# Optimization experiments

Hardware: AMD Instinct MI355X
Metric: run time of the kernel (lower is better)

## Reference

```python
import jax, jax.numpy as jnp
import numpy as np

N_NODES = 50000
N_EDGES = 1600000
F_IN = 384
NR_SIGMOID = 1  # hidden_sizes[-1]


def setup_inputs() -> dict:
    key = jax.random.key(0)
    ks = jax.random.split(key, 8)
    x = jax.random.normal(ks[0], (N_NODES, F_IN), jnp.float32)
    edge_index = jax.random.randint(ks[1], (2, N_EDGES), 0, N_NODES, jnp.int32)
    def lin(k, fin, fout):
        return jax.random.normal(k, (fin, fout), jnp.float32) / np.sqrt(fin).astype(np.float32)
    W1 = lin(ks[2], F_IN, 64)
    W2 = lin(ks[3], 64, 32)
    W3 = lin(ks[4], 32, 1 + F_IN)  # reconstruction=True: last width = 1 + input_size
    return {
        "x": x, "edge_index": edge_index,
        "W1": W1, "b1": jnp.zeros((64,), jnp.float32),
        "W2": W2, "b2": jnp.zeros((32,), jnp.float32),
        "W3": W3, "b3": jnp.zeros((1 + F_IN,), jnp.float32),
    }


def reference(x, edge_index, W1, b1, W2, b2, W3, b3):
    N = x.shape[0]
    self_loop = jnp.arange(N, dtype=edge_index.dtype)
    src = jnp.concatenate([edge_index[0], self_loop])  # [E+N]
    dst = jnp.concatenate([edge_index[1], self_loop])
    # symmetric GCN normalization (with self-loops), as in PyG GCNConv
    deg = jax.ops.segment_sum(jnp.ones(dst.shape[0], x.dtype), dst, num_segments=N)
    dinv = jnp.where(deg > 0, jax.lax.rsqrt(deg), 0.0)
    norm = (dinv[src] * dinv[dst])[:, None]  # [E+N, 1]

    def gcn_conv(h, W, b):
        m = h @ W                         # transform first (fewer message bytes)
        agg = jax.ops.segment_sum(m[src] * norm, dst, num_segments=N)
        return agg + b

    h = jax.nn.relu(gcn_conv(x, W1, b1))
    h = jax.nn.relu(gcn_conv(h, W2, b2))
    h = gcn_conv(h, W3, b3)
    # sigmoid on the first nr_sigmoid_layers columns only
    return jnp.concatenate([jax.nn.sigmoid(h[:, :NR_SIGMOID]), h[:, NR_SIGMOID:]], axis=1)
```

## Files before the change

### kernel.cpp

```cpp
#include <hip/hip_runtime.h>

#define F_IN  384
#define EPB   4096
#define NBINS 256
#define BCAP  10240
#define SDS   208
#define WTBLK 144

typedef __attribute__((ext_vector_type(8))) short short8v;
typedef __attribute__((ext_vector_type(4))) float f32x4;

__device__ __forceinline__ unsigned short f2bf(float f) {
    unsigned u = __float_as_uint(f);
    return (unsigned short)((u + 0x7FFFu + ((u >> 16) & 1u)) >> 16);
}
__device__ __forceinline__ float bflo(unsigned u) { return __uint_as_float(u << 16); }
__device__ __forceinline__ float bfhi(unsigned u) { return __uint_as_float(u & 0xFFFF0000u); }


__launch_bounds__(256)
__global__ void k_p1(const int* __restrict__ ei, int E, int NBK, int NB1,
                     unsigned* __restrict__ packed, unsigned short* __restrict__ segdesc,
                     const float* __restrict__ W1, const float* __restrict__ W3,
                     unsigned short* __restrict__ w1t, unsigned short* __restrict__ w3t) {
    __shared__ unsigned sin[EPB];
    __shared__ unsigned sout[EPB];
    __shared__ int hist[257], cur[256], excl[257];
    const int t = threadIdx.x;

    if (blockIdx.x >= NB1) {
        int idx = (blockIdx.x - NB1) * 256 + t;
        if (idx < 384 * 64) {
            int k = idx >> 6, col = idx & 63;
            w1t[(size_t)col * 384 + k] = f2bf(W1[idx]);
        } else {
            int j = idx - 384 * 64;
            if (j < 384 * 32) {
                int col = j >> 5, k = j & 31;
                w3t[(size_t)col * 32 + k] = f2bf(W3[(size_t)k * 385 + col]);
            }
        }
        return;
    }

    const int e0 = blockIdx.x * EPB;
    const int cnt = min(EPB, E - e0);

    if (t < 256) { hist[t] = 0; cur[t] = 0; }
    if (t == 0) hist[256] = 0;
    __syncthreads();

    for (int i = t; i < cnt; i += 256) {
        int s = ei[e0 + i];
        int d = ei[E + e0 + i];
        sin[i] = ((unsigned)d << 16) | (unsigned)s;
        atomicAdd(&hist[d >> 8], 1);
    }
    __syncthreads();

    if (t < 64) {
        int carry = 0;
        for (int c = 0; c * 64 < NBK; ++c) {
            int idx = c * 64 + t;
            int v = (idx < NBK) ? hist[idx] : 0;
            int x = v;
#pragma unroll
            for (int d = 1; d < 64; d <<= 1) { int y = __shfl_up(x, d, 64); if (t >= d) x += y; }
            if (idx < NBK) excl[idx] = carry + x - v;
            carry += __shfl(x, 63, 64);
        }
        if (t == 0) excl[NBK] = carry;
    }
    __syncthreads();

    for (int i = t; i < cnt; i += 256) {
        unsigned v = sin[i];
        int b = v >> 24;
        int pos = excl[b] + atomicAdd(&cur[b], 1);
        sout[pos] = v;
    }
    __syncthreads();

    for (int i = t; i < cnt; i += 256) packed[(size_t)e0 + i] = sout[i];
    for (int i = t; i <= NBK; i += 256) segdesc[(size_t)blockIdx.x * SDS + i] = (unsigned short)excl[i];
}


__launch_bounds__(256)
__global__ void k_p2(const unsigned* __restrict__ packed, const unsigned short* __restrict__ segdesc,
                     int NB1, unsigned short* __restrict__ eidx,
                     int* __restrict__ rpB, int* __restrict__ rpE,
                     float* __restrict__ dinv, int N) {
    __shared__ unsigned ev[BCAP];
    __shared__ unsigned short se[BCAP];
    __shared__ int lenS[512], offS[513], srcS[512];
    __shared__ int hist[NBINS], cur[NBINS], excl[NBINS + 1];
    const int t = threadIdx.x;
    const int b = blockIdx.x;

    if (t < NBINS) { hist[t] = 0; cur[t] = 0; }
    for (int blk = t; blk < NB1; blk += 256) {
        int s0 = segdesc[(size_t)blk * SDS + b];
        int s1 = segdesc[(size_t)blk * SDS + b + 1];
        lenS[blk] = s1 - s0;
        srcS[blk] = s0;
    }
    __syncthreads();

    if (t < 64) {
        int carry = 0;
        for (int c = 0; c * 64 < NB1; ++c) {
            int idx = c * 64 + t;
            int v = (idx < NB1) ? lenS[idx] : 0;
            int x = v;
#pragma unroll
            for (int d = 1; d < 64; d <<= 1) { int y = __shfl_up(x, d, 64); if (t >= d) x += y; }
            if (idx < NB1) offS[idx] = carry + x - v;
            carry += __shfl(x, 63, 64);
        }
        if (t == 0) offS[NB1 < 512 ? NB1 : 512] = carry;
    }
    __syncthreads();
    const int total = min(offS[NB1 < 512 ? NB1 : 512], BCAP);

    for (int blk = t; blk < NB1; blk += 256) {
        int l = lenS[blk], o = offS[blk];
        if (o + l > BCAP) l = max(0, BCAP - o);
        const unsigned* sp = packed + (size_t)blk * EPB + srcS[blk];
        for (int j = 0; j < l; ++j) ev[o + j] = sp[j];
    }
    __syncthreads();

    for (int i = t; i < total; i += 256) atomicAdd(&hist[(ev[i] >> 16) & 0xFF], 1);
    __syncthreads();

    if (t < 64) {
        int carry = 0;
#pragma unroll
        for (int c = 0; c < 4; ++c) {
            int idx = c * 64 + t;
            int v = hist[idx];
            int x = v;
#pragma unroll
            for (int d = 1; d < 64; d <<= 1) { int y = __shfl_up(x, d, 64); if (t >= d) x += y; }
            excl[idx] = carry + x - v;
            carry += __shfl(x, 63, 64);
        }
        if (t == 0) excl[NBINS] = carry;
    }
    __syncthreads();

    if (t < NBINS) {
        int d = b * NBINS + t;
        if (d < N) {
            int c = hist[t];
            int base = b * BCAP + excl[t];
            rpB[d] = base;
            rpE[d] = base + c;
            dinv[d] = rsqrtf((float)(c + 1));
        }
    }
    for (int i = t; i < total; i += 256) {
        unsigned v = ev[i];
        int l = (v >> 16) & 0xFF;
        int p = excl[l] + atomicAdd(&cur[l], 1);
        se[p] = (unsigned short)(v & 0xFFFF);
    }
    __syncthreads();
    for (int i = t; i < total; i += 256) eidx[(size_t)b * BCAP + i] = se[i];
}


__launch_bounds__(256)
__global__ void k_gemm1(const float* __restrict__ x, const unsigned short* __restrict__ w1t,
                        const float* __restrict__ dinv,
                        unsigned short* __restrict__ m1p, int N) {
    __shared__ __align__(16) unsigned short xb[32][136];
    const int t    = threadIdx.x;
    const int lane = t & 63;
    const int wv   = t >> 6;
    const int lr   = lane & 15;
    const int kg   = lane >> 4;
    const int row0 = blockIdx.x * 32;
    const int col  = (wv << 4) + lr;

    short8v bf[12];
    const unsigned short* wcol = w1t + (size_t)col * 384 + (kg << 3);
#pragma unroll
    for (int c = 0; c < 12; c++)
        bf[c] = *reinterpret_cast<const short8v*>(&wcol[c * 32]);

    int sr[2], sk[2];
    const float* sp[2];
    bool sv[2];
#pragma unroll
    for (int i = 0; i < 2; i++) {
        int g = t + i * 256;
        sr[i] = g >> 4;
        sk[i] = (g & 15) << 3;
        int row = row0 + sr[i];
        sv[i] = (row < N);
        sp[i] = x + (size_t)row * F_IN + sk[i];
    }

    float4 preA0, preA1, preB0, preB1;
    preA0 = sv[0] ? *reinterpret_cast<const float4*>(sp[0])     : make_float4(0, 0, 0, 0);
    preA1 = sv[0] ? *reinterpret_cast<const float4*>(sp[0] + 4) : make_float4(0, 0, 0, 0);
    preB0 = sv[1] ? *reinterpret_cast<const float4*>(sp[1])     : make_float4(0, 0, 0, 0);
    preB1 = sv[1] ? *reinterpret_cast<const float4*>(sp[1] + 4) : make_float4(0, 0, 0, 0);

    f32x4 acc0 = (f32x4){0.f, 0.f, 0.f, 0.f};
    f32x4 acc1 = (f32x4){0.f, 0.f, 0.f, 0.f};

    for (int k0 = 0; k0 < F_IN; k0 += 128) {
        __syncthreads();
        {
            short8v p;
            p[0] = (short)f2bf(preA0.x); p[1] = (short)f2bf(preA0.y);
            p[2] = (short)f2bf(preA0.z); p[3] = (short)f2bf(preA0.w);
            p[4] = (short)f2bf(preA1.x); p[5] = (short)f2bf(preA1.y);
            p[6] = (short)f2bf(preA1.z); p[7] = (short)f2bf(preA1.w);
            *reinterpret_cast<short8v*>(&xb[sr[0]][sk[0]]) = p;
            p[0] = (short)f2bf(preB0.x); p[1] = (short)f2bf(preB0.y);
            p[2] = (short)f2bf(preB0.z); p[3] = (short)f2bf(preB0.w);
            p[4] = (short)f2bf(preB1.x); p[5] = (short)f2bf(preB1.y);
            p[6] = (short)f2bf(preB1.z); p[7] = (short)f2bf(preB1.w);
            *reinterpret_cast<short8v*>(&xb[sr[1]][sk[1]]) = p;
        }
        if (k0 + 128 < F_IN) {
            const float* q0 = sp[0] + k0 + 128;
            const float* q1 = sp[1] + k0 + 128;
            preA0 = sv[0] ? *reinterpret_cast<const float4*>(q0)     : make_float4(0, 0, 0, 0);
            preA1 = sv[0] ? *reinterpret_cast<const float4*>(q0 + 4) : make_float4(0, 0, 0, 0);
            preB0 = sv[1] ? *reinterpret_cast<const float4*>(q1)     : make_float4(0, 0, 0, 0);
            preB1 = sv[1] ? *reinterpret_cast<const float4*>(q1 + 4) : make_float4(0, 0, 0, 0);
        }
        __syncthreads();

#pragma unroll
        for (int kk = 0; kk < 4; kk++) {
            const int c = (k0 >> 5) + kk;
            short8v a0 = *reinterpret_cast<const short8v*>(&xb[lr][(kk << 5) + (kg << 3)]);
            short8v a1 = *reinterpret_cast<const short8v*>(&xb[16 + lr][(kk << 5) + (kg << 3)]);
            acc0 = __builtin_amdgcn_mfma_f32_16x16x32_bf16(a0, bf[c], acc0, 0, 0, 0);
            acc1 = __builtin_amdgcn_mfma_f32_16x16x32_bf16(a1, bf[c], acc1, 0, 0, 0);
        }
    }

    const size_t hbase = (size_t)(col >> 5) * ((size_t)N * 32) + (col & 31);
#pragma unroll
    for (int i = 0; i < 4; i++) {
        int rowA = row0 + (kg << 2) + i;
        if (rowA < N) m1p[hbase + (size_t)rowA * 32] = f2bf(acc0[i] * dinv[rowA]);
        int rowB = row0 + 16 + (kg << 2) + i;
        if (rowB < N) m1p[hbase + (size_t)rowB * 32] = f2bf(acc1[i] * dinv[rowB]);
    }
}


__launch_bounds__(256)
__global__ void k_g64half(const int* __restrict__ rpB, const int* __restrict__ rpE,
                          const unsigned short* __restrict__ eidx,
                          const unsigned* __restrict__ msg,
                          const float* __restrict__ b1h,
                          const float* __restrict__ dinv,
                          unsigned* __restrict__ m1h,
                          int houtoff, int N) {
    int w = blockIdx.x * 16 + (threadIdx.x >> 4);
    if (w >= N) return;
    int f = threadIdx.x & 15;
    int i = rpB[w], e = rpE[w];
    unsigned u = msg[(size_t)w * 16 + f];
    float l0 = bflo(u), h0 = bfhi(u);
    float l1 = 0.f, h1 = 0.f, l2 = 0.f, h2 = 0.f, l3 = 0.f, h3 = 0.f;
    float l4 = 0.f, h4 = 0.f, l5 = 0.f, h5 = 0.f, l6 = 0.f, h6 = 0.f, l7 = 0.f, h7 = 0.f;
    for (; i + 8 <= e; i += 8) {
        unsigned u0 = msg[(size_t)eidx[i]     * 16 + f];
        unsigned u1 = msg[(size_t)eidx[i + 1] * 16 + f];
        unsigned u2 = msg[(size_t)eidx[i + 2] * 16 + f];
        unsigned u3 = msg[(size_t)eidx[i + 3] * 16 + f];
        unsigned u4 = msg[(size_t)eidx[i + 4] * 16 + f];
        unsigned u5 = msg[(size_t)eidx[i + 5] * 16 + f];
        unsigned u6 = msg[(size_t)eidx[i + 6] * 16 + f];
        unsigned u7 = msg[(size_t)eidx[i + 7] * 16 + f];
        l0 += bflo(u0); h0 += bfhi(u0);  l1 += bflo(u1); h1 += bfhi(u1);
        l2 += bflo(u2); h2 += bfhi(u2);  l3 += bflo(u3); h3 += bfhi(u3);
        l4 += bflo(u4); h4 += bfhi(u4);  l5 += bflo(u5); h5 += bfhi(u5);
        l6 += bflo(u6); h6 += bfhi(u6);  l7 += bflo(u7); h7 += bfhi(u7);
    }
    for (; i + 4 <= e; i += 4) {
        unsigned u0 = msg[(size_t)eidx[i]     * 16 + f];
        unsigned u1 = msg[(size_t)eidx[i + 1] * 16 + f];
        unsigned u2 = msg[(size_t)eidx[i + 2] * 16 + f];
        unsigned u3 = msg[(size_t)eidx[i + 3] * 16 + f];
        l0 += bflo(u0); h0 += bfhi(u0);  l1 += bflo(u1); h1 += bfhi(u1);
        l2 += bflo(u2); h2 += bfhi(u2);  l3 += bflo(u3); h3 += bfhi(u3);
    }
    for (; i < e; i++) {
        unsigned u0 = msg[(size_t)eidx[i] * 16 + f];
        l0 += bflo(u0); h0 += bfhi(u0);
    }
    float suml = ((l0 + l1) + (l2 + l3)) + ((l4 + l5) + (l6 + l7));
    float sumh = ((h0 + h1) + (h2 + h3)) + ((h4 + h5) + (h6 + h7));
    float s = dinv[w];
    float hl = fmaxf(suml * s + b1h[(f << 1)], 0.f);
    float hh = fmaxf(sumh * s + b1h[(f << 1) + 1], 0.f);
    m1h[(size_t)w * 32 + houtoff + f] = (unsigned)f2bf(hl) | ((unsigned)f2bf(hh) << 16);
}


__launch_bounds__(256)
__global__ void k_gather32h(const int* __restrict__ rpB, const int* __restrict__ rpE,
                            const unsigned short* __restrict__ eidx,
                            const unsigned* __restrict__ msg,
                            unsigned* __restrict__ outp, int N,
                            const float* __restrict__ bias, const float* __restrict__ dinv) {
    int w = blockIdx.x * 16 + (threadIdx.x >> 4);
    if (w >= N) return;
    int f = threadIdx.x & 15;
    int i = rpB[w], e = rpE[w];
    unsigned u = msg[(size_t)w * 16 + f];
    float l0 = bflo(u), h0 = bfhi(u);
    float l1 = 0.f, h1 = 0.f, l2 = 0.f, h2 = 0.f, l3 = 0.f, h3 = 0.f;
    float l4 = 0.f, h4 = 0.f, l5 = 0.f, h5 = 0.f, l6 = 0.f, h6 = 0.f, l7 = 0.f, h7 = 0.f;
    for (; i + 8 <= e; i += 8) {
        unsigned u0 = msg[(size_t)eidx[i]     * 16 + f];
        unsigned u1 = msg[(size_t)eidx[i + 1] * 16 + f];
        unsigned u2 = msg[(size_t)eidx[i + 2] * 16 + f];
        unsigned u3 = msg[(size_t)eidx[i + 3] * 16 + f];
        unsigned u4 = msg[(size_t)eidx[i + 4] * 16 + f];
        unsigned u5 = msg[(size_t)eidx[i + 5] * 16 + f];
        unsigned u6 = msg[(size_t)eidx[i + 6] * 16 + f];
        unsigned u7 = msg[(size_t)eidx[i + 7] * 16 + f];
        l0 += bflo(u0); h0 += bfhi(u0);  l1 += bflo(u1); h1 += bfhi(u1);
        l2 += bflo(u2); h2 += bfhi(u2);  l3 += bflo(u3); h3 += bfhi(u3);
        l4 += bflo(u4); h4 += bfhi(u4);  l5 += bflo(u5); h5 += bfhi(u5);
        l6 += bflo(u6); h6 += bfhi(u6);  l7 += bflo(u7); h7 += bfhi(u7);
    }
    for (; i + 4 <= e; i += 4) {
        unsigned u0 = msg[(size_t)eidx[i]     * 16 + f];
        unsigned u1 = msg[(size_t)eidx[i + 1] * 16 + f];
        unsigned u2 = msg[(size_t)eidx[i + 2] * 16 + f];
        unsigned u3 = msg[(size_t)eidx[i + 3] * 16 + f];
        l0 += bflo(u0); h0 += bfhi(u0);  l1 += bflo(u1); h1 += bfhi(u1);
        l2 += bflo(u2); h2 += bfhi(u2);  l3 += bflo(u3); h3 += bfhi(u3);
    }
    for (; i < e; i++) {
        unsigned u0 = msg[(size_t)eidx[i] * 16 + f];
        l0 += bflo(u0); h0 += bfhi(u0);
    }
    float rl = ((l0 + l1) + (l2 + l3)) + ((l4 + l5) + (l6 + l7));
    float rh = ((h0 + h1) + (h2 + h3)) + ((h4 + h5) + (h6 + h7));
    float s = dinv[w];
    rl = fmaxf(rl * s + bias[(f << 1)], 0.f) * s;
    rh = fmaxf(rh * s + bias[(f << 1) + 1], 0.f) * s;
    outp[(size_t)w * 16 + f] = (unsigned)f2bf(rl) | ((unsigned)f2bf(rh) << 16);
}


__launch_bounds__(256)
__global__ void k_layer2(const unsigned* __restrict__ m1h, const float* __restrict__ W2,
                         const float* __restrict__ dinv,
                         unsigned short* __restrict__ m2p, int N) {
    const int t    = threadIdx.x;
    const int lane = t & 63;
    const int wv   = t >> 6;
    const int lr   = lane & 15;
    const int kg   = lane >> 4;
    const int row0 = blockIdx.x * 64 + (wv << 4);

    short8v b00, b01, b10, b11;
#pragma unroll
    for (int j = 0; j < 8; j++) {
        int k = (kg << 3) + j;
        b00[j] = (short)f2bf(W2[(size_t)k * 32 + lr]);
        b01[j] = (short)f2bf(W2[(size_t)k * 32 + 16 + lr]);
        b10[j] = (short)f2bf(W2[(size_t)(32 + k) * 32 + lr]);
        b11[j] = (short)f2bf(W2[(size_t)(32 + k) * 32 + 16 + lr]);
    }

    int arow = row0 + lr;
    short8v a0 = (short8v){0, 0, 0, 0, 0, 0, 0, 0};
    short8v a1 = (short8v){0, 0, 0, 0, 0, 0, 0, 0};
    if (arow < N) {
        a0 = *reinterpret_cast<const short8v*>(&m1h[(size_t)arow * 32 + (kg << 2)]);
        a1 = *reinterpret_cast<const short8v*>(&m1h[(size_t)arow * 32 + 16 + (kg << 2)]);
    }

    f32x4 accA = (f32x4){0.f, 0.f, 0.f, 0.f};
    f32x4 accB = (f32x4){0.f, 0.f, 0.f, 0.f};
    accA = __builtin_amdgcn_mfma_f32_16x16x32_bf16(a0, b00, accA, 0, 0, 0);
    accA = __builtin_amdgcn_mfma_f32_16x16x32_bf16(a1, b10, accA, 0, 0, 0);
    accB = __builtin_amdgcn_mfma_f32_16x16x32_bf16(a0, b01, accB, 0, 0, 0);
    accB = __builtin_amdgcn_mfma_f32_16x16x32_bf16(a1, b11, accB, 0, 0, 0);

#pragma unroll
    for (int i = 0; i < 4; i++) {
        int row = row0 + (kg << 2) + i;
        if (row < N) {
            float s = dinv[row];
            m2p[(size_t)row * 32 + lr]      = f2bf(accA[i] * s);
            m2p[(size_t)row * 32 + 16 + lr] = f2bf(accB[i] * s);
        }
    }
}


__launch_bounds__(256)
__global__ void k_g32out(const int* __restrict__ rpB, const int* __restrict__ rpE,
                         const unsigned short* __restrict__ eidx,
                         const uint4* __restrict__ msg,
                         const float* __restrict__ dinv,
                         const unsigned short* __restrict__ w3t,
                         const float* __restrict__ W3, const float* __restrict__ b3,
                         float* __restrict__ out, int N) {
    __shared__ unsigned g[64][16];
    const int t    = threadIdx.x;
    const int row0 = blockIdx.x * 64;
    const int wn   = t >> 2;
    const int q    = t & 3;
    const int w    = row0 + wn;

    if (w < N) {
        int i = rpB[w], e = rpE[w];
        uint4 u = msg[(size_t)w * 4 + q];
        float a0 = bflo(u.x), a1 = bfhi(u.x), a2 = bflo(u.y), a3 = bfhi(u.y);
        float a4 = bflo(u.z), a5 = bfhi(u.z), a6 = bflo(u.w), a7 = bfhi(u.w);
        float c0 = 0.f, c1 = 0.f, c2 = 0.f, c3 = 0.f, c4 = 0.f, c5 = 0.f, c6 = 0.f, c7 = 0.f;
        for (; i + 4 <= e; i += 4) {
            uint4 v0 = msg[(size_t)eidx[i]     * 4 + q];
            uint4 v1 = msg[(size_t)eidx[i + 1] * 4 + q];
            uint4 v2 = msg[(size_t)eidx[i + 2] * 4 + q];
            uint4 v3 = msg[(size_t)eidx[i + 3] * 4 + q];
            a0 += bflo(v0.x); a1 += bfhi(v0.x); a2 += bflo(v0.y); a3 += bfhi(v0.y);
            a4 += bflo(v0.z); a5 += bfhi(v0.z); a6 += bflo(v0.w); a7 += bfhi(v0.w);
            c0 += bflo(v1.x); c1 += bfhi(v1.x); c2 += bflo(v1.y); c3 += bfhi(v1.y);
            c4 += bflo(v1.z); c5 += bfhi(v1.z); c6 += bflo(v1.w); c7 += bfhi(v1.w);
            a0 += bflo(v2.x); a1 += bfhi(v2.x); a2 += bflo(v2.y); a3 += bfhi(v2.y);
            a4 += bflo(v2.z); a5 += bfhi(v2.z); a6 += bflo(v2.w); a7 += bfhi(v2.w);
            c0 += bflo(v3.x); c1 += bfhi(v3.x); c2 += bflo(v3.y); c3 += bfhi(v3.y);
            c4 += bflo(v3.z); c5 += bfhi(v3.z); c6 += bflo(v3.w); c7 += bfhi(v3.w);
        }
        for (; i < e; i++) {
            uint4 v0 = msg[(size_t)eidx[i] * 4 + q];
            a0 += bflo(v0.x); a1 += bfhi(v0.x); a2 += bflo(v0.y); a3 += bfhi(v0.y);
            a4 += bflo(v0.z); a5 += bfhi(v0.z); a6 += bflo(v0.w); a7 += bfhi(v0.w);
        }
        float s = dinv[w];
        float g0 = (a0 + c0) * s, g1 = (a1 + c1) * s, g2 = (a2 + c2) * s, g3 = (a3 + c3) * s;
        float g4 = (a4 + c4) * s, g5 = (a5 + c5) * s, g6 = (a6 + c6) * s, g7 = (a7 + c7) * s;
        g[wn][q * 4 + 0] = (unsigned)f2bf(g0) | ((unsigned)f2bf(g1) << 16);
        g[wn][q * 4 + 1] = (unsigned)f2bf(g2) | ((unsigned)f2bf(g3) << 16);
        g[wn][q * 4 + 2] = (unsigned)f2bf(g4) | ((unsigned)f2bf(g5) << 16);
        g[wn][q * 4 + 3] = (unsigned)f2bf(g6) | ((unsigned)f2bf(g7) << 16);
        const float* wc = W3 + (size_t)(8 * q) * 385 + 384;
        float p = g0 * wc[0] + g1 * wc[385] + g2 * wc[2 * 385] + g3 * wc[3 * 385]
                + g4 * wc[4 * 385] + g5 * wc[5 * 385] + g6 * wc[6 * 385] + g7 * wc[7 * 385];
        p += __shfl_xor(p, 1, 64);
        p += __shfl_xor(p, 2, 64);
        if (q == 0) out[(size_t)w * 385 + 384] = p + b3[384];
    } else {
        g[wn][q * 4 + 0] = 0; g[wn][q * 4 + 1] = 0;
        g[wn][q * 4 + 2] = 0; g[wn][q * 4 + 3] = 0;
    }
    __syncthreads();

    const int lane = t & 63;
    const int wv   = t >> 6;
    const int lr   = lane & 15;
    const int kg   = lane >> 4;
#pragma unroll
    for (int y = 0; y < 6; y++) {
        int col = y * 64 + (wv << 4) + lr;
        short8v bfrag = *reinterpret_cast<const short8v*>(&w3t[(size_t)col * 32 + (kg << 3)]);
        float bias = b3[col];
#pragma unroll
        for (int rb = 0; rb < 4; rb++) {
            short8v afrag = *reinterpret_cast<const short8v*>(&g[(rb << 4) + lr][kg << 2]);
            f32x4 acc = (f32x4){0.f, 0.f, 0.f, 0.f};
            acc = __builtin_amdgcn_mfma_f32_16x16x32_bf16(afrag, bfrag, acc, 0, 0, 0);
#pragma unroll
            for (int i = 0; i < 4; i++) {
                int row = row0 + (rb << 4) + (kg << 2) + i;
                if (row < N) {
                    float v = acc[i] + bias;
                    if (col == 0) v = 1.0f / (1.0f + expf(-v));
                    out[(size_t)row * 385 + col] = v;
                }
            }
        }
    }
}

extern "C" void kernel_launch(void* const* d_in, const int* in_sizes, int n_in,
                              void* d_out, int out_size, void* d_ws, size_t ws_size,
                              hipStream_t stream) {
    const float* x  = (const float*)d_in[0];
    const int*   ei = (const int*)d_in[1];
    const float* W1 = (const float*)d_in[2];
    const float* b1 = (const float*)d_in[3];
    const float* W2 = (const float*)d_in[4];
    const float* b2 = (const float*)d_in[5];
    const float* W3 = (const float*)d_in[6];
    const float* b3 = (const float*)d_in[7];
    float* out = (float*)d_out;

    const int N = in_sizes[0] / F_IN;
    const int E = in_sizes[1] / 2;
    const int NB1 = (E + EPB - 1) / EPB;
    const int NBK = (N + NBINS - 1) / NBINS;

    float* ws   = (float*)d_ws;
    float* dinv = ws;
    float* bufA = ws + N;
    float* bufB = bufA + (size_t)64 * N;
    int*   rpB  = (int*)(bufB + (size_t)64 * N);
    int*   rpE  = rpB + N;
    unsigned short* eidx    = (unsigned short*)(rpE + N);
    unsigned short* segdesc = eidx + (size_t)NBK * BCAP;
    unsigned short* w1t     = segdesc + (size_t)NB1 * SDS;
    unsigned short* w3t     = w1t + (size_t)64 * 384;

    unsigned* packed = (unsigned*)bufA;
    unsigned short* m1p = (unsigned short*)bufA;
    unsigned* m1h = (unsigned*)bufB;
    unsigned short* m2p = (unsigned short*)bufA;
    unsigned short* h2p = (unsigned short*)bufB;

    k_p1<<<NB1 + WTBLK, 256, 0, stream>>>(ei, E, NBK, NB1, packed, segdesc, W1, W3, w1t, w3t);
    k_p2<<<NBK, 256, 0, stream>>>(packed, segdesc, NB1, eidx, rpB, rpE, dinv, N);

    k_gemm1  <<<(N + 31) / 32, 256, 0, stream>>>(x, w1t, dinv, m1p, N);
    k_g64half<<<(N + 15) / 16, 256, 0, stream>>>(rpB, rpE, eidx,
                                                 (const unsigned*)m1p,                    b1,      dinv, m1h,  0, N);
    k_g64half<<<(N + 15) / 16, 256, 0, stream>>>(rpB, rpE, eidx,
                                                 (const unsigned*)(m1p + (size_t)N * 32), b1 + 32, dinv, m1h, 16, N);

    k_layer2  <<<(N + 63) / 64, 256, 0, stream>>>(m1h, W2, dinv, m2p, N);
    k_gather32h<<<(N + 15) / 16, 256, 0, stream>>>(rpB, rpE, eidx, (const unsigned*)m2p,
                                                   (unsigned*)h2p, N, b2, dinv);

    k_g32out<<<(N + 63) / 64, 256, 0, stream>>>(rpB, rpE, eidx, (const uint4*)h2p, dinv,
                                                w3t, W3, b3, out, N);
}
```

Measured before the change: 145.1 us.

## Fuse layer-1 GEMM into edge-partition kernel and apply dinv scaling in bucket pass

The x@W1 GEMM blocks now run in the same launch as the first edge-partition pass and the W3 transpose, so the GEMM overlaps with the sort work and one kernel launch disappears. W1 is converted to bf16 inline per thread instead of through a pre-transposed buffer. Because dinv is not yet available at that point, the second partition kernel rescales the bf16 GEMM output by dinv after computing degrees. That adds a read-modify-write pass over m1p and a second bf16 rounding, and m1p moves to a separate offset so it does not alias the packed edge buffer.

```diff
diff --git a/kernel.cpp b/kernel.cpp
--- a/kernel.cpp
+++ b/kernel.cpp
@@ -5,7 +5,7 @@
 #define NBINS 256
 #define BCAP  10240
 #define SDS   208
-#define WTBLK 144
+#define WT3B  48
 
 typedef __attribute__((ext_vector_type(8))) short short8v;
 typedef __attribute__((ext_vector_type(4))) float f32x4;
@@ -17,44 +17,125 @@
 __device__ __forceinline__ float bflo(unsigned u) { return __uint_as_float(u << 16); }
 __device__ __forceinline__ float bfhi(unsigned u) { return __uint_as_float(u & 0xFFFF0000u); }
 
+struct SharedP1 { unsigned sin[EPB]; unsigned sout[EPB]; int hist[257], cur[256], excl[257]; };
+struct SharedG1 { unsigned short xb[32][136]; };
+union SharedFront { SharedP1 p; SharedG1 g; };
+
 
 __launch_bounds__(256)
-__global__ void k_p1(const int* __restrict__ ei, int E, int NBK, int NB1,
-                     unsigned* __restrict__ packed, unsigned short* __restrict__ segdesc,
-                     const float* __restrict__ W1, const float* __restrict__ W3,
-                     unsigned short* __restrict__ w1t, unsigned short* __restrict__ w3t) {
-    __shared__ unsigned sin[EPB];
-    __shared__ unsigned sout[EPB];
-    __shared__ int hist[257], cur[256], excl[257];
-    const int t = threadIdx.x;
-
-    if (blockIdx.x >= NB1) {
-        int idx = (blockIdx.x - NB1) * 256 + t;
-        if (idx < 384 * 64) {
-            int k = idx >> 6, col = idx & 63;
-            w1t[(size_t)col * 384 + k] = f2bf(W1[idx]);
-        } else {
-            int j = idx - 384 * 64;
-            if (j < 384 * 32) {
-                int col = j >> 5, k = j & 31;
-                w3t[(size_t)col * 32 + k] = f2bf(W3[(size_t)k * 385 + col]);
+__global__ void k_front(const int* __restrict__ ei, int E, int NBK, int NB1,
+                        unsigned* __restrict__ packed, unsigned short* __restrict__ segdesc,
+                        const float* __restrict__ W1, const float* __restrict__ W3,
+                        unsigned short* __restrict__ w3t,
+                        const float* __restrict__ x, unsigned short* __restrict__ m1p, int N) {
+    __shared__ SharedFront sh;
+    const int t   = threadIdx.x;
+    const int bid = blockIdx.x;
+
+    if (bid >= NB1 + WT3B) {
+        const int lane = t & 63;
+        const int wv   = t >> 6;
+        const int lr   = lane & 15;
+        const int kg   = lane >> 4;
+        const int row0 = (bid - NB1 - WT3B) * 32;
+        const int col  = (wv << 4) + lr;
+
+        short8v bf[12];
+#pragma unroll
+        for (int c = 0; c < 12; c++)
+#pragma unroll
+            for (int j = 0; j < 8; j++)
+                bf[c][j] = (short)f2bf(W1[(size_t)(c * 32 + (kg << 3) + j) * 64 + col]);
+
+        int sr[2], sk[2];
+        const float* sp[2];
+        bool sv[2];
+#pragma unroll
+        for (int i = 0; i < 2; i++) {
+            int g = t + i * 256;
+            sr[i] = g >> 4;
+            sk[i] = (g & 15) << 3;
+            int row = row0 + sr[i];
+            sv[i] = (row < N);
+            sp[i] = x + (size_t)row * F_IN + sk[i];
+        }
+
+        float4 preA0, preA1, preB0, preB1;
+        preA0 = sv[0] ? *reinterpret_cast<const float4*>(sp[0])     : make_float4(0, 0, 0, 0);
+        preA1 = sv[0] ? *reinterpret_cast<const float4*>(sp[0] + 4) : make_float4(0, 0, 0, 0);
+        preB0 = sv[1] ? *reinterpret_cast<const float4*>(sp[1])     : make_float4(0, 0, 0, 0);
+        preB1 = sv[1] ? *reinterpret_cast<const float4*>(sp[1] + 4) : make_float4(0, 0, 0, 0);
+
+        f32x4 acc0 = (f32x4){0.f, 0.f, 0.f, 0.f};
+        f32x4 acc1 = (f32x4){0.f, 0.f, 0.f, 0.f};
+
+        for (int k0 = 0; k0 < F_IN; k0 += 128) {
+            __syncthreads();
+            {
+                short8v p;
+                p[0] = (short)f2bf(preA0.x); p[1] = (short)f2bf(preA0.y);
+                p[2] = (short)f2bf(preA0.z); p[3] = (short)f2bf(preA0.w);
+                p[4] = (short)f2bf(preA1.x); p[5] = (short)f2bf(preA1.y);
+                p[6] = (short)f2bf(preA1.z); p[7] = (short)f2bf(preA1.w);
+                *reinterpret_cast<short8v*>(&sh.g.xb[sr[0]][sk[0]]) = p;
+                p[0] = (short)f2bf(preB0.x); p[1] = (short)f2bf(preB0.y);
+                p[2] = (short)f2bf(preB0.z); p[3] = (short)f2bf(preB0.w);
+                p[4] = (short)f2bf(preB1.x); p[5] = (short)f2bf(preB1.y);
+                p[6] = (short)f2bf(preB1.z); p[7] = (short)f2bf(preB1.w);
+                *reinterpret_cast<short8v*>(&sh.g.xb[sr[1]][sk[1]]) = p;
             }
+            if (k0 + 128 < F_IN) {
+                const float* q0 = sp[0] + k0 + 128;
+                const float* q1 = sp[1] + k0 + 128;
+                preA0 = sv[0] ? *reinterpret_cast<const float4*>(q0)     : make_float4(0, 0, 0, 0);
+                preA1 = sv[0] ? *reinterpret_cast<const float4*>(q0 + 4) : make_float4(0, 0, 0, 0);
+                preB0 = sv[1] ? *reinterpret_cast<const float4*>(q1)     : make_float4(0, 0, 0, 0);
+                preB1 = sv[1] ? *reinterpret_cast<const float4*>(q1 + 4) : make_float4(0, 0, 0, 0);
+            }
+            __syncthreads();
+
+#pragma unroll
+            for (int kk = 0; kk < 4; kk++) {
+                const int c = (k0 >> 5) + kk;
+                short8v a0 = *reinterpret_cast<const short8v*>(&sh.g.xb[lr][(kk << 5) + (kg << 3)]);
+                short8v a1 = *reinterpret_cast<const short8v*>(&sh.g.xb[16 + lr][(kk << 5) + (kg << 3)]);
+                acc0 = __builtin_amdgcn_mfma_f32_16x16x32_bf16(a0, bf[c], acc0, 0, 0, 0);
+                acc1 = __builtin_amdgcn_mfma_f32_16x16x32_bf16(a1, bf[c], acc1, 0, 0, 0);
+            }
+        }
+
+        const size_t hbase = (size_t)(col >> 5) * ((size_t)N * 32) + (col & 31);
+#pragma unroll
+        for (int i = 0; i < 4; i++) {
+            int rowA = row0 + (kg << 2) + i;
+            if (rowA < N) m1p[hbase + (size_t)rowA * 32] = f2bf(acc0[i]);
+            int rowB = row0 + 16 + (kg << 2) + i;
+            if (rowB < N) m1p[hbase + (size_t)rowB * 32] = f2bf(acc1[i]);
         }
         return;
     }
 
-    const int e0 = blockIdx.x * EPB;
+    if (bid >= NB1) {
+        int j = (bid - NB1) * 256 + t;
+        if (j < 384 * 32) {
+            int col = j >> 5, k = j & 31;
+            w3t[(size_t)col * 32 + k] = f2bf(W3[(size_t)k * 385 + col]);
+        }
+        return;
+    }
+
+    const int e0 = bid * EPB;
     const int cnt = min(EPB, E - e0);
 
-    if (t < 256) { hist[t] = 0; cur[t] = 0; }
-    if (t == 0) hist[256] = 0;
+    if (t < 256) { sh.p.hist[t] = 0; sh.p.cur[t] = 0; }
+    if (t == 0) sh.p.hist[256] = 0;
     __syncthreads();
 
     for (int i = t; i < cnt; i += 256) {
         int s = ei[e0 + i];
         int d = ei[E + e0 + i];
-        sin[i] = ((unsigned)d << 16) | (unsigned)s;
-        atomicAdd(&hist[d >> 8], 1);
+        sh.p.sin[i] = ((unsigned)d << 16) | (unsigned)s;
+        atomicAdd(&sh.p.hist[d >> 8], 1);
     }
     __syncthreads();
 
@@ -62,27 +143,27 @@
         int carry = 0;
         for (int c = 0; c * 64 < NBK; ++c) {
             int idx = c * 64 + t;
-            int v = (idx < NBK) ? hist[idx] : 0;
-            int x = v;
-#pragma unroll
-            for (int d = 1; d < 64; d <<= 1) { int y = __shfl_up(x, d, 64); if (t >= d) x += y; }
-            if (idx < NBK) excl[idx] = carry + x - v;
-            carry += __shfl(x, 63, 64);
-        }
-        if (t == 0) excl[NBK] = carry;
+            int v = (idx < NBK) ? sh.p.hist[idx] : 0;
+            int x2 = v;
+#pragma unroll
+            for (int d = 1; d < 64; d <<= 1) { int y = __shfl_up(x2, d, 64); if (t >= d) x2 += y; }
+            if (idx < NBK) sh.p.excl[idx] = carry + x2 - v;
+            carry += __shfl(x2, 63, 64);
+        }
+        if (t == 0) sh.p.excl[NBK] = carry;
     }
     __syncthreads();
 
     for (int i = t; i < cnt; i += 256) {
-        unsigned v = sin[i];
+        unsigned v = sh.p.sin[i];
         int b = v >> 24;
-        int pos = excl[b] + atomicAdd(&cur[b], 1);
-        sout[pos] = v;
-    }
-    __syncthreads();
-
-    for (int i = t; i < cnt; i += 256) packed[(size_t)e0 + i] = sout[i];
-    for (int i = t; i <= NBK; i += 256) segdesc[(size_t)blockIdx.x * SDS + i] = (unsigned short)excl[i];
+        int pos = sh.p.excl[b] + atomicAdd(&sh.p.cur[b], 1);
+        sh.p.sout[pos] = v;
+    }
+    __syncthreads();
+
+    for (int i = t; i < cnt; i += 256) packed[(size_t)e0 + i] = sh.p.sout[i];
+    for (int i = t; i <= NBK; i += 256) segdesc[(size_t)bid * SDS + i] = (unsigned short)sh.p.excl[i];
 }
 
 
@@ -90,7 +171,7 @@
 __global__ void k_p2(const unsigned* __restrict__ packed, const unsigned short* __restrict__ segdesc,
                      int NB1, unsigned short* __restrict__ eidx,
                      int* __restrict__ rpB, int* __restrict__ rpE,
-                     float* __restrict__ dinv, int N) {
+                     float* __restrict__ dinv, unsigned* __restrict__ m1p32, int N) {
     __shared__ unsigned ev[BCAP];
     __shared__ unsigned short se[BCAP];
     __shared__ int lenS[512], offS[513], srcS[512];
@@ -168,92 +249,18 @@
     }
     __syncthreads();
     for (int i = t; i < total; i += 256) eidx[(size_t)b * BCAP + i] = se[i];
-}
-
-
-__launch_bounds__(256)
-__global__ void k_gemm1(const float* __restrict__ x, const unsigned short* __restrict__ w1t,
-                        const float* __restrict__ dinv,
-                        unsigned short* __restrict__ m1p, int N) {
-    __shared__ __align__(16) unsigned short xb[32][136];
-    const int t    = threadIdx.x;
-    const int lane = t & 63;
-    const int wv   = t >> 6;
-    const int lr   = lane & 15;
-    const int kg   = lane >> 4;
-    const int row0 = blockIdx.x * 32;
-    const int col  = (wv << 4) + lr;
-
-    short8v bf[12];
-    const unsigned short* wcol = w1t + (size_t)col * 384 + (kg << 3);
-#pragma unroll
-    for (int c = 0; c < 12; c++)
-        bf[c] = *reinterpret_cast<const short8v*>(&wcol[c * 32]);
-
-    int sr[2], sk[2];
-    const float* sp[2];
-    bool sv[2];
-#pragma unroll
-    for (int i = 0; i < 2; i++) {
-        int g = t + i * 256;
-        sr[i] = g >> 4;
-        sk[i] = (g & 15) << 3;
-        int row = row0 + sr[i];
-        sv[i] = (row < N);
-        sp[i] = x + (size_t)row * F_IN + sk[i];
-    }
-
-    float4 preA0, preA1, preB0, preB1;
-    preA0 = sv[0] ? *reinterpret_cast<const float4*>(sp[0])     : make_float4(0, 0, 0, 0);
-    preA1 = sv[0] ? *reinterpret_cast<const float4*>(sp[0] + 4) : make_float4(0, 0, 0, 0);
-    preB0 = sv[1] ? *reinterpret_cast<const float4*>(sp[1])     : make_float4(0, 0, 0, 0);
-    preB1 = sv[1] ? *reinterpret_cast<const float4*>(sp[1] + 4) : make_float4(0, 0, 0, 0);
-
-    f32x4 acc0 = (f32x4){0.f, 0.f, 0.f, 0.f};
-    f32x4 acc1 = (f32x4){0.f, 0.f, 0.f, 0.f};
-
-    for (int k0 = 0; k0 < F_IN; k0 += 128) {
-        __syncthreads();
-        {
-            short8v p;
-            p[0] = (short)f2bf(preA0.x); p[1] = (short)f2bf(preA0.y);
-            p[2] = (short)f2bf(preA0.z); p[3] = (short)f2bf(preA0.w);
-            p[4] = (short)f2bf(preA1.x); p[5] = (short)f2bf(preA1.y);
-            p[6] = (short)f2bf(preA1.z); p[7] = (short)f2bf(preA1.w);
-            *reinterpret_cast<short8v*>(&xb[sr[0]][sk[0]]) = p;
-            p[0] = (short)f2bf(preB0.x); p[1] = (short)f2bf(preB0.y);
-            p[2] = (short)f2bf(preB0.z); p[3] = (short)f2bf(preB0.w);
-            p[4] = (short)f2bf(preB1.x); p[5] = (short)f2bf(preB1.y);
-            p[6] = (short)f2bf(preB1.z); p[7] = (short)f2bf(preB1.w);
-            *reinterpret_cast<short8v*>(&xb[sr[1]][sk[1]]) = p;
-        }
-        if (k0 + 128 < F_IN) {
-            const float* q0 = sp[0] + k0 + 128;
-            const float* q1 = sp[1] + k0 + 128;
-            preA0 = sv[0] ? *reinterpret_cast<const float4*>(q0)     : make_float4(0, 0, 0, 0);
-            preA1 = sv[0] ? *reinterpret_cast<const float4*>(q0 + 4) : make_float4(0, 0, 0, 0);
-            preB0 = sv[1] ? *reinterpret_cast<const float4*>(q1)     : make_float4(0, 0, 0, 0);
-            preB1 = sv[1] ? *reinterpret_cast<const float4*>(q1 + 4) : make_float4(0, 0, 0, 0);
-        }
-        __syncthreads();
-
-#pragma unroll
-        for (int kk = 0; kk < 4; kk++) {
-            const int c = (k0 >> 5) + kk;
-            short8v a0 = *reinterpret_cast<const short8v*>(&xb[lr][(kk << 5) + (kg << 3)]);
-            short8v a1 = *reinterpret_cast<const short8v*>(&xb[16 + lr][(kk << 5) + (kg << 3)]);
-            acc0 = __builtin_amdgcn_mfma_f32_16x16x32_bf16(a0, bf[c], acc0, 0, 0, 0);
-            acc1 = __builtin_amdgcn_mfma_f32_16x16x32_bf16(a1, bf[c], acc1, 0, 0, 0);
-        }
-    }
-
-    const size_t hbase = (size_t)(col >> 5) * ((size_t)N * 32) + (col & 31);
-#pragma unroll
-    for (int i = 0; i < 4; i++) {
-        int rowA = row0 + (kg << 2) + i;
-        if (rowA < N) m1p[hbase + (size_t)rowA * 32] = f2bf(acc0[i] * dinv[rowA]);
-        int rowB = row0 + 16 + (kg << 2) + i;
-        if (rowB < N) m1p[hbase + (size_t)rowB * 32] = f2bf(acc1[i] * dinv[rowB]);
+
+    for (int i = t; i < NBINS * 16 * 2; i += 256) {
+        int h = i >> 12;
+        int r = (i >> 4) & 255;
+        int f = i & 15;
+        int d = b * NBINS + r;
+        if (d < N) {
+            float s = rsqrtf((float)(hist[r] + 1));
+            size_t idx = (size_t)h * N * 16 + (size_t)d * 16 + f;
+            unsigned v = m1p32[idx];
+            m1p32[idx] = (unsigned)f2bf(bflo(v) * s) | ((unsigned)f2bf(bfhi(v) * s) << 16);
+        }
     }
 }
 
@@ -509,6 +516,7 @@
     const int E = in_sizes[1] / 2;
     const int NB1 = (E + EPB - 1) / EPB;
     const int NBK = (N + NBINS - 1) / NBINS;
+    const int NGB = (N + 31) / 32;
 
     float* ws   = (float*)d_ws;
     float* dinv = ws;
@@ -518,23 +526,23 @@
     int*   rpE  = rpB + N;
     unsigned short* eidx    = (unsigned short*)(rpE + N);
     unsigned short* segdesc = eidx + (size_t)NBK * BCAP;
-    unsigned short* w1t     = segdesc + (size_t)NB1 * SDS;
-    unsigned short* w3t     = w1t + (size_t)64 * 384;
+    unsigned short* w3t     = segdesc + (size_t)NB1 * SDS;
 
     unsigned* packed = (unsigned*)bufA;
-    unsigned short* m1p = (unsigned short*)bufA;
+    unsigned short* m1p = (unsigned short*)(bufA + (size_t)32 * N);
     unsigned* m1h = (unsigned*)bufB;
     unsigned short* m2p = (unsigned short*)bufA;
     unsigned short* h2p = (unsigned short*)bufB;
 
-    k_p1<<<NB1 + WTBLK, 256, 0, stream>>>(ei, E, NBK, NB1, packed, segdesc, W1, W3, w1t, w3t);
-    k_p2<<<NBK, 256, 0, stream>>>(packed, segdesc, NB1, eidx, rpB, rpE, dinv, N);
-
-    k_gemm1  <<<(N + 31) / 32, 256, 0, stream>>>(x, w1t, dinv, m1p, N);
+    k_front<<<NB1 + WT3B + NGB, 256, 0, stream>>>(ei, E, NBK, NB1, packed, segdesc,
+                                                  W1, W3, w3t, x, m1p, N);
+    k_p2<<<NBK, 256, 0, stream>>>(packed, segdesc, NB1, eidx, rpB, rpE, dinv,
+                                  (unsigned*)m1p, N);
+
     k_g64half<<<(N + 15) / 16, 256, 0, stream>>>(rpB, rpE, eidx,
                                                  (const unsigned*)m1p,                    b1,      dinv, m1h,  0, N);
     k_g64half<<<(N + 15) / 16, 256, 0, stream>>>(rpB, rpE, eidx,
-                                                 (const unsigned*)(m1p + (size_t)N * 32), b1 + 32, dinv, m1h, 16, N);
+                                                 (const unsigned*)m1p + (size_t)N * 16,   b1 + 32, dinv, m1h, 16, N);
 
     k_layer2  <<<(N + 63) / 64, 256, 0, stream>>>(m1h, W2, dinv, m2p, N);
     k_gather32h<<<(N + 15) / 16, 256, 0, stream>>>(rpB, rpE, eidx, (const unsigned*)m2p,
```

Result: slower. 149.1 us (+2.7%).
